# Optimization experiments

Measured on AMD Instinct MI355X. Metric: run time of the kernel, lower is better.

The kernel has to match this reference:

```python
import jax, jax.numpy as jnp
import numpy as np

B, C, H, W, E, R, TOP_K = 8, 128, 128, 128, 4, 64, 2


def setup_inputs() -> dict:
    key = jax.random.key(0)
    ks = jax.random.split(key, 12)
    s = 0.02
    return {
        "x": jax.random.normal(ks[0], (B, C, H, W), jnp.float32),
        "shared": jax.random.normal(ks[1], (B, C, H, W), jnp.float32),
        # FrequencyEmbedding MLP: Linear(C,2C) -> GELU -> Linear(2C,C)
        "mlp_w1": jax.random.normal(ks[2], (C, 2 * C), jnp.float32) * s,
        "mlp_b1": jnp.zeros((2 * C,), jnp.float32),
        "mlp_w2": jax.random.normal(ks[3], (2 * C, C), jnp.float32) * s,
        "mlp_b2": jnp.zeros((C,), jnp.float32),
        # routing gates: Linear(C,E) on pooled x, Linear(C,E) on freq emb
        "gate_w": jax.random.normal(ks[4], (C, E), jnp.float32) * s,
        "freq_gate_w": jax.random.normal(ks[5], (C, E), jnp.float32) * s,
        # per-expert 1x1 conv weights (ModExpert.proj, expert_layer=Identity)
        "exp_w0": jax.random.normal(ks[6], (E, R, C), jnp.float32) * s,  # dim->rank
        "exp_w1": jax.random.normal(ks[7], (E, R, C), jnp.float32) * s,  # dim->rank (on shared)
        "exp_w2": jax.random.normal(ks[8], (E, C, R), jnp.float32) * s,  # rank->dim
        # AdapterLayer.proj_out 1x1 conv
        "proj_w": jax.random.normal(ks[9], (C, C), jnp.float32) * s,
    }


def reference(x, shared, mlp_w1, mlp_b1, mlp_w2, mlp_b2, gate_w, freq_gate_w,
              exp_w0, exp_w1, exp_w2, proj_w):
    b, c = x.shape[0], x.shape[1]
    # --- FrequencyEmbedding: frozen depthwise high-pass 3x3 -> GELU -> mean(HW) -> MLP ---
    hp = jnp.array([[-1., -1., -1.], [-1., 8., -1.], [-1., -1., -1.]], dtype=x.dtype)
    kern = jnp.broadcast_to(hp, (c, 1, 3, 3))
    h = jax.lax.conv_general_dilated(
        x, kern, window_strides=(1, 1), padding='SAME',
        feature_group_count=c, dimension_numbers=('NCHW', 'OIHW', 'NCHW'))
    h = jax.nn.gelu(h, approximate=False)
    fe = h.mean(axis=(-2, -1))                                    # [B, C]
    fe = jax.nn.gelu(fe @ mlp_w1 + mlp_b1, approximate=False) @ mlp_w2 + mlp_b2
    # --- RoutingFunction (eval / noiseless): softmax -> top-k -> scatter gates ---
    pooled = x.mean(axis=(-2, -1))                                # [B, C]
    logits = pooled @ gate_w + fe @ freq_gate_w                   # [B, E]
    scores = jax.nn.softmax(logits, axis=-1)
    vals, idx = jax.lax.top_k(scores, TOP_K)
    gates = jnp.zeros_like(scores).at[jnp.arange(b)[:, None], idx].set(vals)  # [B, E]
    # --- Experts (dense equivalent of SparseDispatcher gather->expert->scatter-add) ---
    # expert_e(x, shared) = x + W2_e @ ((W0_e @ x) * silu(W1_e @ shared))
    a = jnp.einsum('bchw,erc->berhw', x, exp_w0)                  # [B,E,R,H,W]
    g = jax.nn.silu(jnp.einsum('bchw,erc->berhw', shared, exp_w1))
    y = jnp.einsum('berhw,edr->bedhw', a * g, exp_w2)             # [B,E,C,H,W]
    # gated combine; residual shortcut enters once per selected expert, weighted by gate
    out = jnp.einsum('be,bedhw->bdhw', gates, y) + gates.sum(axis=1)[:, None, None, None] * x
    # --- proj_out 1x1 ---
    return jnp.einsum('bchw,dc->bdhw', out, proj_w)
```

## Files before the change

### kernel.cpp

```cpp
#include <hip/hip_runtime.h>
#include <hip/hip_bf16.h>
#include <math.h>

#define CC   128
#define HWN  16384
#define EE   4
#define RR   64
#define TP   64
#define NT   (HWN / TP)

typedef __attribute__((ext_vector_type(8))) short short8;
typedef __attribute__((ext_vector_type(4))) float f32x4;

__device__ __forceinline__ unsigned short f2bf(float f) {
    __hip_bfloat16 h = __float2bfloat16(f);
    return *reinterpret_cast<unsigned short*>(&h);
}
__device__ __forceinline__ unsigned pk2bf(float lo, float hi) {
    return (unsigned)f2bf(lo) | ((unsigned)f2bf(hi) << 16);
}
__device__ __forceinline__ float gelu_exact(float v) {
    return 0.5f * v * (1.0f + erff(v * 0.7071067811865475f));
}
__device__ __forceinline__ float silu_f(float v) {
    return v / (1.0f + expf(-v));
}

#define PREP_CVX  512
#define PREP_SHP  (PREP_CVX + 512)
#define PREP_WCV  (PREP_SHP + 128)
#define PREP_WF   (PREP_WCV + 128)
#define PREP_GRID (PREP_WF + 48)
__global__ __launch_bounds__(256) void k_prep(
    const float* __restrict__ x,   const float* __restrict__ sh,
    const float* __restrict__ proj,
    const float* __restrict__ ew0, const float* __restrict__ ew1,
    const float* __restrict__ ew2,
    const float* __restrict__ mw1, const float* __restrict__ mw2,
    const float* __restrict__ gw,  const float* __restrict__ fgw,
    float* __restrict__ fe0, float* __restrict__ pooled,
    unsigned short* __restrict__ projb, unsigned short* __restrict__ w0b,
    unsigned short* __restrict__ w1b,   unsigned short* __restrict__ w2pb,
    float* __restrict__ outw, float* __restrict__ dummy)
{
    __shared__ float wr2[2][2][4];
    const int bx = blockIdx.x, tid = threadIdx.x;

    if (bx < PREP_CVX) {
        const int dpr  = bx & 63;
        const int b    = bx >> 6;
        const int ln   = tid & 63;
        const int wv   = tid >> 6;
        const int half = ln >> 5;
        const int c4   = (ln & 31) << 2;
        const float* src = x + ((size_t)(b * CC + 2 * dpr + half)) * HWN + c4;
        unsigned* dst = (unsigned*)outw + ((size_t)(b * CC + dpr)) * HWN + c4;
        const int r0 = wv << 5;

        const float4 z4 = {0.f, 0.f, 0.f, 0.f};
        float4 t4 = z4, m4, b4;
        float tl = 0.f, tr = 0.f, ml, mr, bl, br;
        if (r0 > 0) {
            t4 = *(const float4*)(src + (size_t)(r0 - 1) * 128);
            tl = __shfl(t4.w, ln - 1, 64); if ((ln & 31) == 0)  tl = 0.f;
            tr = __shfl(t4.x, ln + 1, 64); if ((ln & 31) == 31) tr = 0.f;
        }
        m4 = *(const float4*)(src + (size_t)r0 * 128);
        ml = __shfl(m4.w, ln - 1, 64); if ((ln & 31) == 0)  ml = 0.f;
        mr = __shfl(m4.x, ln + 1, 64); if ((ln & 31) == 31) mr = 0.f;

        float sg = 0.f, sx = 0.f;
        for (int g = r0; g < r0 + 32; ++g) {
            if (g + 1 < 128) {
                b4 = *(const float4*)(src + (size_t)(g + 1) * 128);
                bl = __shfl(b4.w, ln - 1, 64); if ((ln & 31) == 0)  bl = 0.f;
                br = __shfl(b4.x, ln + 1, 64); if ((ln & 31) == 31) br = 0.f;
            } else { b4 = z4; bl = 0.f; br = 0.f; }
            const float ta[6] = {tl, t4.x, t4.y, t4.z, t4.w, tr};
            const float ma[6] = {ml, m4.x, m4.y, m4.z, m4.w, mr};
            const float ba[6] = {bl, b4.x, b4.y, b4.z, b4.w, br};
            #pragma unroll
            for (int k = 0; k < 4; ++k) {
                float s8 = ((ta[k] + ta[k+1]) + (ta[k+2] + ma[k]))
                         + ((ma[k+2] + ba[k]) + (ba[k+1] + ba[k+2]));
                sg += gelu_exact(8.f * ma[k+1] - s8);
                sx += ma[k+1];
            }
            float ox = __shfl(m4.x, ln ^ 32, 64);
            float oy = __shfl(m4.y, ln ^ 32, 64);
            float oz = __shfl(m4.z, ln ^ 32, 64);
            float ow = __shfl(m4.w, ln ^ 32, 64);
            if (half == 0) {
                uint4 w;
                w.x = pk2bf(m4.x, ox); w.y = pk2bf(m4.y, oy);
                w.z = pk2bf(m4.z, oz); w.w = pk2bf(m4.w, ow);
                *(uint4*)(dst + (size_t)g * 128) = w;
            }
            t4 = m4; tl = ml; tr = mr;
            m4 = b4; ml = bl; mr = br;
        }
        #pragma unroll
        for (int off = 16; off; off >>= 1) {
            sg += __shfl_xor(sg, off, 64);
            sx += __shfl_xor(sx, off, 64);
        }
        if ((ln & 31) == 0) { wr2[half][0][wv] = sg; wr2[half][1][wv] = sx; }
        __syncthreads();
        if (tid < 2) {
            float g4 = (wr2[tid][0][0] + wr2[tid][0][1]) + (wr2[tid][0][2] + wr2[tid][0][3]);
            float x4 = (wr2[tid][1][0] + wr2[tid][1][1]) + (wr2[tid][1][2] + wr2[tid][1][3]);
            fe0   [b * CC + 2 * dpr + tid] = g4 * (1.f / 16384.f);
            pooled[b * CC + 2 * dpr + tid] = x4 * (1.f / 16384.f);
        }
    } else if (bx < PREP_SHP) {
        const int idx = bx - PREP_CVX;
        const int dpr = idx & 63;
        const int b   = idx >> 6;
        const float* s0 = sh + ((size_t)b * CC + 2 * dpr) * HWN;
        const float4* a4 = (const float4*)s0;
        const float4* c4p = (const float4*)(s0 + HWN);
        uint4* dst = (uint4*)((unsigned*)outw + ((size_t)(b * CC + 64 + dpr)) * HWN);
        for (int i = tid; i < HWN / 4; i += 256) {
            float4 a = a4[i], c = c4p[i];
            uint4 w;
            w.x = pk2bf(a.x, c.x);
            w.y = pk2bf(a.y, c.y);
            w.z = pk2bf(a.z, c.z);
            w.w = pk2bf(a.w, c.w);
            dst[i] = w;
        }
    } else if (bx < PREP_WCV) {
        int i = (bx - PREP_SHP) * 256 + tid;
        if (i < CC * CC) projb[i] = f2bf(proj[i]);
        w0b[i] = f2bf(ew0[i]);
        w1b[i] = f2bf(ew1[i]);
    } else if (bx < PREP_WF) {
        const int bb = bx - PREP_WCV;
        const int e  = bb >> 5;
        const int d  = ((bb & 31) << 2) + (tid >> 6);
        const int r  = tid & 63;
        const float* pr = proj + d * CC;
        const float* wz = ew2 + (size_t)e * CC * RR + r;
        float a0 = 0.f, a1 = 0.f, a2 = 0.f, a3 = 0.f;
        for (int c = 0; c < CC; c += 4) {
            a0 += pr[c + 0] * wz[(c + 0) * RR];
            a1 += pr[c + 1] * wz[(c + 1) * RR];
            a2 += pr[c + 2] * wz[(c + 2) * RR];
            a3 += pr[c + 3] * wz[(c + 3) * RR];
        }
        w2pb[(e * CC + d) * RR + r] = f2bf((a0 + a1) + (a2 + a3));
    } else {
        const int i = (bx - PREP_WF) * 256 + tid;
        float s = 0.f;
        for (int j = i; j < CC * 2 * CC; j += 48 * 256) s += mw1[j] + mw2[j];
        if (i < CC * EE) s += gw[i] + fgw[i];
        if (s == 12345.678f) dummy[1] = s;
    }
}

__global__ __launch_bounds__(256) void k_route(
    const float* __restrict__ fe0, const float* __restrict__ pooled,
    const float* __restrict__ w1, const float* __restrict__ b1,
    const float* __restrict__ w2, const float* __restrict__ b2,
    const float* __restrict__ gw, const float* __restrict__ fgw,
    float* __restrict__ gates, float* __restrict__ gsum)
{
    const int b = blockIdx.x, tid = threadIdx.x;
    __shared__ float hh[256];
    __shared__ float fe[128];
    __shared__ float lg[4];
    {
        const float* f0 = fe0 + b * CC;
        float a[8];
        #pragma unroll
        for (int j = 0; j < 8; ++j) a[j] = 0.f;
        for (int c = 0; c < CC; c += 8)
            #pragma unroll
            for (int j = 0; j < 8; ++j) a[j] += f0[c + j] * w1[(c + j) * 256 + tid];
        float acc = b1[tid] + ((a[0]+a[1]) + (a[2]+a[3])) + ((a[4]+a[5]) + (a[6]+a[7]));
        hh[tid] = gelu_exact(acc);
    }
    __syncthreads();
    if (tid < 128) {
        float a[8];
        #pragma unroll
        for (int j = 0; j < 8; ++j) a[j] = 0.f;
        for (int c = 0; c < 256; c += 8)
            #pragma unroll
            for (int j = 0; j < 8; ++j) a[j] += hh[c + j] * w2[(c + j) * 128 + tid];
        fe[tid] = b2[tid] + ((a[0]+a[1]) + (a[2]+a[3])) + ((a[4]+a[5]) + (a[6]+a[7]));
    }
    __syncthreads();
    if (tid < EE) {
        const float* pl = pooled + b * CC;
        float l0=0.f, l1=0.f, l2=0.f, l3=0.f;
        for (int c = 0; c < CC; c += 4) {
            l0 += pl[c+0] * gw[(c+0) * EE + tid] + fe[c+0] * fgw[(c+0) * EE + tid];
            l1 += pl[c+1] * gw[(c+1) * EE + tid] + fe[c+1] * fgw[(c+1) * EE + tid];
            l2 += pl[c+2] * gw[(c+2) * EE + tid] + fe[c+2] * fgw[(c+2) * EE + tid];
            l3 += pl[c+3] * gw[(c+3) * EE + tid] + fe[c+3] * fgw[(c+3) * EE + tid];
        }
        lg[tid] = (l0 + l1) + (l2 + l3);
    }
    __syncthreads();
    if (tid == 0) {
        float mx = fmaxf(fmaxf(lg[0], lg[1]), fmaxf(lg[2], lg[3]));
        float sc[EE]; float ssum = 0.f;
        for (int e = 0; e < EE; ++e) { sc[e] = expf(lg[e] - mx); ssum += sc[e]; }
        float inv = 1.f / ssum;
        for (int e = 0; e < EE; ++e) sc[e] *= inv;
        int i1 = 0;
        for (int e = 1; e < EE; ++e) if (sc[e] > sc[i1]) i1 = e;
        int i2 = -1;
        for (int e = 0; e < EE; ++e) {
            if (e == i1) continue;
            if (i2 < 0 || sc[e] > sc[i2]) i2 = e;
        }
        for (int e = 0; e < EE; ++e)
            gates[b * EE + e] = (e == i1) ? sc[i1] : (e == i2 ? sc[i2] : 0.f);
        gsum[b] = sc[i1] + sc[i2];
    }
}

__global__ __launch_bounds__(256, 4) void k_experts(
    const unsigned short* __restrict__ w0b, const unsigned short* __restrict__ w1b,
    const unsigned short* __restrict__ w2pb, const unsigned short* __restrict__ projb,
    const float* __restrict__ gates, const float* __restrict__ gsum,
    float* __restrict__ out)
{
    __shared__ __align__(16) unsigned short xs [TP * CC];
    __shared__ __align__(16) unsigned short shs[TP * CC];
    __shared__ __align__(16) unsigned short us [TP * RR];
    const int tid  = threadIdx.x;
    const int b    = blockIdx.x >> 8;
    const int tile = blockIdx.x & (NT - 1);
    const int p0   = tile * TP;

    {
        const unsigned* wsrc = (const unsigned*)out + ((size_t)b * CC) * HWN + p0;
        const int p  = tid & 63;
        const int qh = tid >> 6;
        #pragma unroll
        for (int it = 0; it < 4; ++it) {
            const int q  = it * 4 + qh;
            const int sw = p * CC + ((q ^ (p & 15)) << 3);
            const unsigned* px_ = wsrc + (size_t)(q * 4) * HWN + p;
            const unsigned* ps_ = wsrc + (size_t)(64 + q * 4) * HWN + p;
            uint4 wx, wh;
            wx.x = px_[0]; wx.y = px_[HWN]; wx.z = px_[2 * HWN]; wx.w = px_[3 * HWN];
            wh.x = ps_[0]; wh.y = ps_[HWN]; wh.z = ps_[2 * HWN]; wh.w = ps_[3 * HWN];
            *(uint4*)&xs [sw] = wx;
            *(uint4*)&shs[sw] = wh;
        }
    }
    __syncthreads();

    const int wv = tid >> 6;
    const int ln = tid & 63;
    const int lp = ln & 15;
    const int lq = ln >> 4;

    f32x4 acc[2][4];
    #pragma unroll
    for (int i = 0; i < 2; ++i)
        #pragma unroll
        for (int j = 0; j < 4; ++j) acc[i][j] = (f32x4){0.f, 0.f, 0.f, 0.f};

    {
        const int d0 = wv * 32;
        #pragma unroll
        for (int ks = 0; ks < 4; ++ks) {
            const int k0 = ks * 32 + lq * 8;
            const int ch = ks * 4 + lq;
            short8 a0 = *(const short8*)&projb[(d0 +      lp) * CC + k0];
            short8 a1 = *(const short8*)&projb[(d0 + 16 + lp) * CC + k0];
            #pragma unroll
            for (int pt = 0; pt < 4; ++pt) {
                short8 bf = *(const short8*)&xs[(pt * 16 + lp) * CC + ((ch ^ lp) << 3)];
                acc[0][pt] = __builtin_amdgcn_mfma_f32_16x16x32_bf16(a0, bf, acc[0][pt], 0, 0, 0);
                acc[1][pt] = __builtin_amdgcn_mfma_f32_16x16x32_bf16(a1, bf, acc[1][pt], 0, 0, 0);
            }
        }
        const float gs = gsum[b];
        #pragma unroll
        for (int i = 0; i < 2; ++i)
            #pragma unroll
            for (int j = 0; j < 4; ++j) acc[i][j] *= gs;
    }

    for (int e = 0; e < EE; ++e) {
        const float ge = gates[b * EE + e];
        if (ge == 0.f) continue;

        f32x4 af[4], gf[4];
        #pragma unroll
        for (int pt = 0; pt < 4; ++pt) { af[pt] = (f32x4){0.f,0.f,0.f,0.f}; gf[pt] = (f32x4){0.f,0.f,0.f,0.f}; }
        const unsigned short* w0e = w0b + (size_t)(e * RR + wv * 16) * CC;
        const unsigned short* w1e = w1b + (size_t)(e * RR + wv * 16) * CC;
        #pragma unroll
        for (int ks = 0; ks < 4; ++ks) {
            const int k0 = ks * 32 + lq * 8;
            const int ch = ks * 4 + lq;
            short8 a0 = *(const short8*)&w0e[lp * CC + k0];
            short8 a1 = *(const short8*)&w1e[lp * CC + k0];
            #pragma unroll
            for (int pt = 0; pt < 4; ++pt) {
                const int sw = (pt * 16 + lp) * CC + ((ch ^ lp) << 3);
                short8 bx = *(const short8*)&xs [sw];
                short8 bs = *(const short8*)&shs[sw];
                af[pt] = __builtin_amdgcn_mfma_f32_16x16x32_bf16(a0, bx, af[pt], 0, 0, 0);
                gf[pt] = __builtin_amdgcn_mfma_f32_16x16x32_bf16(a1, bs, gf[pt], 0, 0, 0);
            }
        }
        __syncthreads();
        #pragma unroll
        for (int pt = 0; pt < 4; ++pt) {
            unsigned short t[4];
            #pragma unroll
            for (int i = 0; i < 4; ++i)
                t[i] = f2bf(ge * af[pt][i] * silu_f(gf[pt][i]));
            const int p = pt * 16 + lp;
            const int addr = p * RR + (((wv * 2 + (lq >> 1)) ^ (lp & 7)) << 3) + ((lq & 1) << 2);
            *(uint2*)&us[addr] = *(uint2*)t;
        }
        __syncthreads();
        const unsigned short* w2e = w2pb + (size_t)(e * CC + wv * 32) * RR;
        #pragma unroll
        for (int ks = 0; ks < 2; ++ks) {
            const int k0 = ks * 32 + lq * 8;
            const int ch = ks * 4 + lq;
            short8 a0 = *(const short8*)&w2e[lp * RR + k0];
            short8 a1 = *(const short8*)&w2e[(16 + lp) * RR + k0];
            #pragma unroll
            for (int pt = 0; pt < 4; ++pt) {
                short8 bu = *(const short8*)&us[(pt * 16 + lp) * RR + ((ch ^ (lp & 7)) << 3)];
                acc[0][pt] = __builtin_amdgcn_mfma_f32_16x16x32_bf16(a0, bu, acc[0][pt], 0, 0, 0);
                acc[1][pt] = __builtin_amdgcn_mfma_f32_16x16x32_bf16(a1, bu, acc[1][pt], 0, 0, 0);
            }
        }
    }

    {
        const int d0 = wv * 32;
        #pragma unroll
        for (int dt = 0; dt < 2; ++dt)
            #pragma unroll
            for (int pt = 0; pt < 4; ++pt) {
                float* ob = out + ((size_t)(b * CC + d0 + dt * 16 + lq * 4)) * HWN + p0 + pt * 16 + lp;
                #pragma unroll
                for (int i = 0; i < 4; ++i)
                    ob[(size_t)i * HWN] = acc[dt][pt][i];
            }
    }
}

extern "C" void kernel_launch(void* const* d_in, const int* in_sizes, int n_in,
                              void* d_out, int out_size, void* d_ws, size_t ws_size,
                              hipStream_t stream) {
    const float* x    = (const float*)d_in[0];
    const float* shr  = (const float*)d_in[1];
    const float* mw1  = (const float*)d_in[2];
    const float* mb1  = (const float*)d_in[3];
    const float* mw2  = (const float*)d_in[4];
    const float* mb2  = (const float*)d_in[5];
    const float* gw   = (const float*)d_in[6];
    const float* fgw  = (const float*)d_in[7];
    const float* ew0  = (const float*)d_in[8];
    const float* ew1  = (const float*)d_in[9];
    const float* ew2  = (const float*)d_in[10];
    const float* pw   = (const float*)d_in[11];
    float* out = (float*)d_out;

    float* ws     = (float*)d_ws;
    float* fe0    = ws + 0;
    float* pooled = ws + 1024;
    float* gates  = ws + 2048;
    float* gsum   = ws + 2080;
    float* dummy  = ws + 2088;
    unsigned short* projb = (unsigned short*)(ws + 2112);
    unsigned short* w0b   = projb + 16384;
    unsigned short* w1b   = w0b + 32768;
    unsigned short* w2pb  = w1b + 32768;

    k_prep   <<<PREP_GRID, 256, 0, stream>>>(x, shr, pw, ew0, ew1, ew2, mw1, mw2,
                                             gw, fgw, fe0, pooled, projb, w0b, w1b, w2pb,
                                             out, dummy);
    k_route  <<<8,         256, 0, stream>>>(fe0, pooled, mw1, mb1, mw2, mb2, gw, fgw, gates, gsum);
    k_experts<<<8 * NT,    256, 0, stream>>>(w0b, w1b, w2pb, projb, gates, gsum, out);
}
```

Baseline: 259.4 us.

## Split conv prep into row bands, merge shared-pack work into conv blocks

The conv/pool prep now splits each channel pair into two row bands across 1024 blocks. Each wave-half processes both channels over 8 rows, so the half-wave shuffle and predicated store for bf16 packing go away. The separate shared-tensor packing blocks are folded into the same blocks, and each band writes partial sums that k_route adds together. The aim is more parallelism and shorter serial row loops in the memory-bound prep kernel, at the cost of extra halo row loads per band and more registers per thread, now under launch_bounds(256,4).

```diff
diff --git a/kernel.cpp b/kernel.cpp
--- a/kernel.cpp
+++ b/kernel.cpp
@@ -26,111 +26,133 @@
     return v / (1.0f + expf(-v));
 }
 
-#define PREP_CVX  512
-#define PREP_SHP  (PREP_CVX + 512)
-#define PREP_WCV  (PREP_SHP + 128)
+#define PREP_CONV 1024
+#define PREP_WCV  (PREP_CONV + 128)
 #define PREP_WF   (PREP_WCV + 128)
 #define PREP_GRID (PREP_WF + 48)
-__global__ __launch_bounds__(256) void k_prep(
+__global__ __launch_bounds__(256, 4) void k_prep(
     const float* __restrict__ x,   const float* __restrict__ sh,
     const float* __restrict__ proj,
     const float* __restrict__ ew0, const float* __restrict__ ew1,
     const float* __restrict__ ew2,
     const float* __restrict__ mw1, const float* __restrict__ mw2,
     const float* __restrict__ gw,  const float* __restrict__ fgw,
-    float* __restrict__ fe0, float* __restrict__ pooled,
+    float* __restrict__ fe0p, float* __restrict__ poolp,
     unsigned short* __restrict__ projb, unsigned short* __restrict__ w0b,
     unsigned short* __restrict__ w1b,   unsigned short* __restrict__ w2pb,
     float* __restrict__ outw, float* __restrict__ dummy)
 {
-    __shared__ float wr2[2][2][4];
+    __shared__ float wr[8][4];
     const int bx = blockIdx.x, tid = threadIdx.x;
 
-    if (bx < PREP_CVX) {
-        const int dpr  = bx & 63;
-        const int b    = bx >> 6;
+    if (bx < PREP_CONV) {
+        const int b    = bx >> 7;
+        const int dpr  = (bx & 127) >> 1;
+        const int band = bx & 1;
         const int ln   = tid & 63;
         const int wv   = tid >> 6;
         const int half = ln >> 5;
-        const int c4   = (ln & 31) << 2;
-        const float* src = x + ((size_t)(b * CC + 2 * dpr + half)) * HWN + c4;
+        const int l    = ln & 31;
+        const int c4   = l << 2;
+        const int strm = wv * 2 + half;
+        const int r0   = band * 64 + strm * 8;
+
+        const float* srcA = x + ((size_t)(b * CC + 2 * dpr)) * HWN + c4;
+        const float* srcB = srcA + HWN;
         unsigned* dst = (unsigned*)outw + ((size_t)(b * CC + dpr)) * HWN + c4;
-        const int r0 = wv << 5;
 
         const float4 z4 = {0.f, 0.f, 0.f, 0.f};
-        float4 t4 = z4, m4, b4;
-        float tl = 0.f, tr = 0.f, ml, mr, bl, br;
+        float4 tA = z4, tB = z4, mA, mB, bA = z4, bB = z4;
+        float tlA = 0.f, trA = 0.f, tlB = 0.f, trB = 0.f;
+        float mlA, mrA, mlB, mrB, blA = 0.f, brA = 0.f, blB = 0.f, brB = 0.f;
         if (r0 > 0) {
-            t4 = *(const float4*)(src + (size_t)(r0 - 1) * 128);
-            tl = __shfl(t4.w, ln - 1, 64); if ((ln & 31) == 0)  tl = 0.f;
-            tr = __shfl(t4.x, ln + 1, 64); if ((ln & 31) == 31) tr = 0.f;
-        }
-        m4 = *(const float4*)(src + (size_t)r0 * 128);
-        ml = __shfl(m4.w, ln - 1, 64); if ((ln & 31) == 0)  ml = 0.f;
-        mr = __shfl(m4.x, ln + 1, 64); if ((ln & 31) == 31) mr = 0.f;
-
-        float sg = 0.f, sx = 0.f;
-        for (int g = r0; g < r0 + 32; ++g) {
+            tA = *(const float4*)(srcA + (size_t)(r0 - 1) * 128);
+            tB = *(const float4*)(srcB + (size_t)(r0 - 1) * 128);
+            tlA = __shfl(tA.w, ln - 1, 64); if (l == 0)  tlA = 0.f;
+            trA = __shfl(tA.x, ln + 1, 64); if (l == 31) trA = 0.f;
+            tlB = __shfl(tB.w, ln - 1, 64); if (l == 0)  tlB = 0.f;
+            trB = __shfl(tB.x, ln + 1, 64); if (l == 31) trB = 0.f;
+        }
+        mA = *(const float4*)(srcA + (size_t)r0 * 128);
+        mB = *(const float4*)(srcB + (size_t)r0 * 128);
+        mlA = __shfl(mA.w, ln - 1, 64); if (l == 0)  mlA = 0.f;
+        mrA = __shfl(mA.x, ln + 1, 64); if (l == 31) mrA = 0.f;
+        mlB = __shfl(mB.w, ln - 1, 64); if (l == 0)  mlB = 0.f;
+        mrB = __shfl(mB.x, ln + 1, 64); if (l == 31) mrB = 0.f;
+
+        float sgA = 0.f, sxA = 0.f, sgB = 0.f, sxB = 0.f;
+        for (int g = r0; g < r0 + 8; ++g) {
             if (g + 1 < 128) {
-                b4 = *(const float4*)(src + (size_t)(g + 1) * 128);
-                bl = __shfl(b4.w, ln - 1, 64); if ((ln & 31) == 0)  bl = 0.f;
-                br = __shfl(b4.x, ln + 1, 64); if ((ln & 31) == 31) br = 0.f;
-            } else { b4 = z4; bl = 0.f; br = 0.f; }
-            const float ta[6] = {tl, t4.x, t4.y, t4.z, t4.w, tr};
-            const float ma[6] = {ml, m4.x, m4.y, m4.z, m4.w, mr};
-            const float ba[6] = {bl, b4.x, b4.y, b4.z, b4.w, br};
-            #pragma unroll
-            for (int k = 0; k < 4; ++k) {
-                float s8 = ((ta[k] + ta[k+1]) + (ta[k+2] + ma[k]))
-                         + ((ma[k+2] + ba[k]) + (ba[k+1] + ba[k+2]));
-                sg += gelu_exact(8.f * ma[k+1] - s8);
-                sx += ma[k+1];
-            }
-            float ox = __shfl(m4.x, ln ^ 32, 64);
-            float oy = __shfl(m4.y, ln ^ 32, 64);
-            float oz = __shfl(m4.z, ln ^ 32, 64);
-            float ow = __shfl(m4.w, ln ^ 32, 64);
-            if (half == 0) {
+                bA = *(const float4*)(srcA + (size_t)(g + 1) * 128);
+                bB = *(const float4*)(srcB + (size_t)(g + 1) * 128);
+                blA = __shfl(bA.w, ln - 1, 64); if (l == 0)  blA = 0.f;
+                brA = __shfl(bA.x, ln + 1, 64); if (l == 31) brA = 0.f;
+                blB = __shfl(bB.w, ln - 1, 64); if (l == 0)  blB = 0.f;
+                brB = __shfl(bB.x, ln + 1, 64); if (l == 31) brB = 0.f;
+            } else { bA = z4; bB = z4; blA = brA = blB = brB = 0.f; }
+            {
+                const float ta[6] = {tlA, tA.x, tA.y, tA.z, tA.w, trA};
+                const float ma[6] = {mlA, mA.x, mA.y, mA.z, mA.w, mrA};
+                const float ba[6] = {blA, bA.x, bA.y, bA.z, bA.w, brA};
+                #pragma unroll
+                for (int k = 0; k < 4; ++k) {
+                    float s8 = ((ta[k] + ta[k+1]) + (ta[k+2] + ma[k]))
+                             + ((ma[k+2] + ba[k]) + (ba[k+1] + ba[k+2]));
+                    sgA += gelu_exact(8.f * ma[k+1] - s8);
+                    sxA += ma[k+1];
+                }
+            }
+            {
+                const float ta[6] = {tlB, tB.x, tB.y, tB.z, tB.w, trB};
+                const float ma[6] = {mlB, mB.x, mB.y, mB.z, mB.w, mrB};
+                const float ba[6] = {blB, bB.x, bB.y, bB.z, bB.w, brB};
+                #pragma unroll
+                for (int k = 0; k < 4; ++k) {
+                    float s8 = ((ta[k] + ta[k+1]) + (ta[k+2] + ma[k]))
+                             + ((ma[k+2] + ba[k]) + (ba[k+1] + ba[k+2]));
+                    sgB += gelu_exact(8.f * ma[k+1] - s8);
+                    sxB += ma[k+1];
+                }
+            }
+            uint4 w;
+            w.x = pk2bf(mA.x, mB.x); w.y = pk2bf(mA.y, mB.y);
+            w.z = pk2bf(mA.z, mB.z); w.w = pk2bf(mA.w, mB.w);
+            *(uint4*)(dst + (size_t)g * 128) = w;
+            tA = mA; tlA = mlA; trA = mrA; mA = bA; mlA = blA; mrA = brA;
+            tB = mB; tlB = mlB; trB = mrB; mB = bB; mlB = blB; mrB = brB;
+        }
+        #pragma unroll
+        for (int off = 16; off; off >>= 1) {
+            sgA += __shfl_xor(sgA, off, 64); sxA += __shfl_xor(sxA, off, 64);
+            sgB += __shfl_xor(sgB, off, 64); sxB += __shfl_xor(sxB, off, 64);
+        }
+        if (l == 0) { wr[strm][0] = sgA; wr[strm][1] = sxA; wr[strm][2] = sgB; wr[strm][3] = sxB; }
+        __syncthreads();
+        if (tid < 4) {
+            float s = 0.f;
+            #pragma unroll
+            for (int q = 0; q < 8; ++q) s += wr[q][tid];
+            s *= (1.f / 16384.f);
+            const int o = band * 1024 + b * CC + 2 * dpr;
+            if (tid == 0) fe0p [o]     = s;
+            if (tid == 1) poolp[o]     = s;
+            if (tid == 2) fe0p [o + 1] = s;
+            if (tid == 3) poolp[o + 1] = s;
+        }
+        {
+            const float4* a4  = (const float4*)(sh + ((size_t)(b * CC + 2 * dpr)) * HWN + band * 8192);
+            const float4* c4p = (const float4*)(sh + ((size_t)(b * CC + 2 * dpr + 1)) * HWN + band * 8192);
+            uint4* dsts = (uint4*)((unsigned*)outw + ((size_t)(b * CC + 64 + dpr)) * HWN + band * 8192);
+            for (int i = tid; i < 2048; i += 256) {
+                float4 a = a4[i], c = c4p[i];
                 uint4 w;
-                w.x = pk2bf(m4.x, ox); w.y = pk2bf(m4.y, oy);
-                w.z = pk2bf(m4.z, oz); w.w = pk2bf(m4.w, ow);
-                *(uint4*)(dst + (size_t)g * 128) = w;
-            }
-            t4 = m4; tl = ml; tr = mr;
-            m4 = b4; ml = bl; mr = br;
-        }
-        #pragma unroll
-        for (int off = 16; off; off >>= 1) {
-            sg += __shfl_xor(sg, off, 64);
-            sx += __shfl_xor(sx, off, 64);
-        }
-        if ((ln & 31) == 0) { wr2[half][0][wv] = sg; wr2[half][1][wv] = sx; }
-        __syncthreads();
-        if (tid < 2) {
-            float g4 = (wr2[tid][0][0] + wr2[tid][0][1]) + (wr2[tid][0][2] + wr2[tid][0][3]);
-            float x4 = (wr2[tid][1][0] + wr2[tid][1][1]) + (wr2[tid][1][2] + wr2[tid][1][3]);
-            fe0   [b * CC + 2 * dpr + tid] = g4 * (1.f / 16384.f);
-            pooled[b * CC + 2 * dpr + tid] = x4 * (1.f / 16384.f);
-        }
-    } else if (bx < PREP_SHP) {
-        const int idx = bx - PREP_CVX;
-        const int dpr = idx & 63;
-        const int b   = idx >> 6;
-        const float* s0 = sh + ((size_t)b * CC + 2 * dpr) * HWN;
-        const float4* a4 = (const float4*)s0;
-        const float4* c4p = (const float4*)(s0 + HWN);
-        uint4* dst = (uint4*)((unsigned*)outw + ((size_t)(b * CC + 64 + dpr)) * HWN);
-        for (int i = tid; i < HWN / 4; i += 256) {
-            float4 a = a4[i], c = c4p[i];
-            uint4 w;
-            w.x = pk2bf(a.x, c.x);
-            w.y = pk2bf(a.y, c.y);
-            w.z = pk2bf(a.z, c.z);
-            w.w = pk2bf(a.w, c.w);
-            dst[i] = w;
+                w.x = pk2bf(a.x, c.x); w.y = pk2bf(a.y, c.y);
+                w.z = pk2bf(a.z, c.z); w.w = pk2bf(a.w, c.w);
+                dsts[i] = w;
+            }
         }
     } else if (bx < PREP_WCV) {
-        int i = (bx - PREP_SHP) * 256 + tid;
+        int i = (bx - PREP_CONV) * 256 + tid;
         if (i < CC * CC) projb[i] = f2bf(proj[i]);
         w0b[i] = f2bf(ew0[i]);
         w1b[i] = f2bf(ew1[i]);
@@ -159,7 +181,7 @@
 }
 
 __global__ __launch_bounds__(256) void k_route(
-    const float* __restrict__ fe0, const float* __restrict__ pooled,
+    const float* __restrict__ fe0p, const float* __restrict__ poolp,
     const float* __restrict__ w1, const float* __restrict__ b1,
     const float* __restrict__ w2, const float* __restrict__ b2,
     const float* __restrict__ gw, const float* __restrict__ fgw,
@@ -170,13 +192,14 @@
     __shared__ float fe[128];
     __shared__ float lg[4];
     {
-        const float* f0 = fe0 + b * CC;
+        const float* f0 = fe0p + b * CC;
+        const float* f1 = fe0p + 1024 + b * CC;
         float a[8];
         #pragma unroll
         for (int j = 0; j < 8; ++j) a[j] = 0.f;
         for (int c = 0; c < CC; c += 8)
             #pragma unroll
-            for (int j = 0; j < 8; ++j) a[j] += f0[c + j] * w1[(c + j) * 256 + tid];
+            for (int j = 0; j < 8; ++j) a[j] += (f0[c + j] + f1[c + j]) * w1[(c + j) * 256 + tid];
         float acc = b1[tid] + ((a[0]+a[1]) + (a[2]+a[3])) + ((a[4]+a[5]) + (a[6]+a[7]));
         hh[tid] = gelu_exact(acc);
     }
@@ -192,13 +215,14 @@
     }
     __syncthreads();
     if (tid < EE) {
-        const float* pl = pooled + b * CC;
+        const float* pl0 = poolp + b * CC;
+        const float* pl1 = poolp + 1024 + b * CC;
         float l0=0.f, l1=0.f, l2=0.f, l3=0.f;
         for (int c = 0; c < CC; c += 4) {
-            l0 += pl[c+0] * gw[(c+0) * EE + tid] + fe[c+0] * fgw[(c+0) * EE + tid];
-            l1 += pl[c+1] * gw[(c+1) * EE + tid] + fe[c+1] * fgw[(c+1) * EE + tid];
-            l2 += pl[c+2] * gw[(c+2) * EE + tid] + fe[c+2] * fgw[(c+2) * EE + tid];
-            l3 += pl[c+3] * gw[(c+3) * EE + tid] + fe[c+3] * fgw[(c+3) * EE + tid];
+            l0 += (pl0[c+0]+pl1[c+0]) * gw[(c+0) * EE + tid] + fe[c+0] * fgw[(c+0) * EE + tid];
+            l1 += (pl0[c+1]+pl1[c+1]) * gw[(c+1) * EE + tid] + fe[c+1] * fgw[(c+1) * EE + tid];
+            l2 += (pl0[c+2]+pl1[c+2]) * gw[(c+2) * EE + tid] + fe[c+2] * fgw[(c+2) * EE + tid];
+            l3 += (pl0[c+3]+pl1[c+3]) * gw[(c+3) * EE + tid] + fe[c+3] * fgw[(c+3) * EE + tid];
         }
         lg[tid] = (l0 + l1) + (l2 + l3);
     }
@@ -372,19 +396,19 @@
     float* out = (float*)d_out;
 
     float* ws     = (float*)d_ws;
-    float* fe0    = ws + 0;
-    float* pooled = ws + 1024;
-    float* gates  = ws + 2048;
-    float* gsum   = ws + 2080;
-    float* dummy  = ws + 2088;
-    unsigned short* projb = (unsigned short*)(ws + 2112);
+    float* fe0p   = ws + 0;
+    float* poolp  = ws + 2048;
+    float* gates  = ws + 4096;
+    float* gsum   = ws + 4128;
+    float* dummy  = ws + 4136;
+    unsigned short* projb = (unsigned short*)(ws + 4160);
     unsigned short* w0b   = projb + 16384;
     unsigned short* w1b   = w0b + 32768;
     unsigned short* w2pb  = w1b + 32768;
 
     k_prep   <<<PREP_GRID, 256, 0, stream>>>(x, shr, pw, ew0, ew1, ew2, mw1, mw2,
-                                             gw, fgw, fe0, pooled, projb, w0b, w1b, w2pb,
+                                             gw, fgw, fe0p, poolp, projb, w0b, w1b, w2pb,
                                              out, dummy);
-    k_route  <<<8,         256, 0, stream>>>(fe0, pooled, mw1, mb1, mw2, mb2, gw, fgw, gates, gsum);
+    k_route  <<<8,         256, 0, stream>>>(fe0p, poolp, mw1, mb1, mw2, mb2, gw, fgw, gates, gsum);
     k_experts<<<8 * NT,    256, 0, stream>>>(w0b, w1b, w2pb, projb, gates, gsum, out);
 }
```

New measurement: 253.8 us. 2.2% less time.
